# Performance work log

Hardware: AMD Instinct MI355X
Metric: run time of the kernel (lower is better)

The kernel has to match this reference:

```python
import jax, jax.numpy as jnp
import numpy as np


def setup_inputs() -> dict:
    key = jax.random.key(0)
    x = jax.random.normal(key, (8, 2048, 512), dtype=jnp.float32)
    return {"x": x}


def reference(x):
    # x: [B, S, D]; unscaled causal self-attention with Q=K=V=x
    B, S, D = x.shape
    scores = jnp.einsum('bsd,btd->bst', x, x)  # [B, S, S]
    causal = jnp.tril(jnp.ones((S, S), dtype=bool))  # True where allowed
    scores = jnp.where(causal[None, :, :], scores, -jnp.inf)
    attn = jax.nn.softmax(scores, axis=-1)
    out = jnp.einsum('bst,btd->bsd', attn, x)  # [B, S, D]
    return out
```

## Files before the change

### kernel.cpp

```cpp
#include <hip/hip_runtime.h>


#define S_LEN 2048
#define D_DIM 512
#define BATCH_ELEMS 1048576

typedef short s16x8 __attribute__((ext_vector_type(8)));
typedef float f32x4 __attribute__((ext_vector_type(4)));

__device__ __forceinline__ unsigned short f2b_rne(float f) {
  unsigned int u = __float_as_uint(f);
  return (unsigned short)((u + 0x7FFFu + ((u >> 16) & 1u)) >> 16);
}
__device__ __forceinline__ unsigned short f2b_fast(float f) {
  return (unsigned short)((__float_as_uint(f) + 0x8000u) >> 16);
}

template <int CTRL>
__device__ __forceinline__ float dppf(float x) {
  return __uint_as_float((unsigned)__builtin_amdgcn_update_dpp(
      0, (int)__float_as_uint(x), CTRL, 0xF, 0xF, true));
}
__device__ __forceinline__ float red16_max(float v) {
  v = fmaxf(v, dppf<0xB1>(v));
  v = fmaxf(v, dppf<0x4E>(v));
  v = fmaxf(v, dppf<0x124>(v));
  v = fmaxf(v, dppf<0x128>(v));
  return v;
}
__device__ __forceinline__ float red16_sum(float v) {
  v += dppf<0xB1>(v);
  v += dppf<0x4E>(v);
  v += dppf<0x124>(v);
  v += dppf<0x128>(v);
  return v;
}

__global__ void pack_kernel(const float* __restrict__ x,
                            unsigned short* __restrict__ Kf,
                            unsigned short* __restrict__ Vf) {
  __shared__ unsigned short A[64 * 72];
  __shared__ unsigned short T[64 * 72];
  const int bid = blockIdx.x;
  const int b = bid >> 8, rem = bid & 255;
  const int s0 = (rem >> 3) * 64, d0 = (rem & 7) * 64;
  const int tid = threadIdx.x;

  #pragma unroll
  for (int it = 0; it < 2; ++it) {
    int slot = it * 256 + tid;
    int row = slot >> 3, c = slot & 7;
    const float* src = x + ((size_t)(b * S_LEN + s0 + row)) * D_DIM + d0 + c * 8;
    const float4 v0 = *(const float4*)(src);
    const float4 v1 = *(const float4*)(src + 4);
    s16x8 o;
    o[0] = (short)f2b_rne(v0.x); o[1] = (short)f2b_rne(v0.y);
    o[2] = (short)f2b_rne(v0.z); o[3] = (short)f2b_rne(v0.w);
    o[4] = (short)f2b_rne(v1.x); o[5] = (short)f2b_rne(v1.y);
    o[6] = (short)f2b_rne(v1.z); o[7] = (short)f2b_rne(v1.w);
    *(s16x8*)&A[row * 72 + c * 8] = o;
  }
  __syncthreads();

  {
    int sr = tid >> 4, sc = tid & 15;
    ushort4 a0 = *(const ushort4*)&A[(4 * sr + 0) * 72 + 4 * sc];
    ushort4 a1 = *(const ushort4*)&A[(4 * sr + 1) * 72 + 4 * sc];
    ushort4 a2 = *(const ushort4*)&A[(4 * sr + 2) * 72 + 4 * sc];
    ushort4 a3 = *(const ushort4*)&A[(4 * sr + 3) * 72 + 4 * sc];
    ushort4 t0; t0.x = a0.x; t0.y = a1.x; t0.z = a2.x; t0.w = a3.x;
    ushort4 t1; t1.x = a0.y; t1.y = a1.y; t1.z = a2.y; t1.w = a3.y;
    ushort4 t2; t2.x = a0.z; t2.y = a1.z; t2.z = a2.z; t2.w = a3.z;
    ushort4 t3; t3.x = a0.w; t3.y = a1.w; t3.z = a2.w; t3.w = a3.w;
    *(ushort4*)&T[(4 * sc + 0) * 72 + 4 * sr] = t0;
    *(ushort4*)&T[(4 * sc + 1) * 72 + 4 * sr] = t1;
    *(ushort4*)&T[(4 * sc + 2) * 72 + 4 * sr] = t2;
    *(ushort4*)&T[(4 * sc + 3) * 72 + 4 * sr] = t3;
  }
  __syncthreads();

  #pragma unroll
  for (int it = 0; it < 2; ++it) {
    int slot = it * 256 + tid;
    int frag = slot >> 6;
    int lane = slot & 63;
    int l15 = lane & 15, quad = lane >> 4;
    int f1 = frag >> 1, f0 = frag & 1;
    {
      s16x8 val = *(const s16x8*)&A[(f1 * 16 + l15) * 72 + f0 * 32 + quad * 8];
      size_t kg = (size_t)(s0 >> 4) + f1, db = (size_t)(d0 >> 5) + f0;
      *(s16x8*)(Kf + (size_t)b * BATCH_ELEMS + (kg * 16 + db) * 512 + lane * 8) = val;
    }
    {
      s16x8 val = *(const s16x8*)&T[(f1 * 16 + l15) * 72 + f0 * 32 + quad * 8];
      size_t dg = (size_t)(d0 >> 4) + f1, kb = (size_t)(s0 >> 5) + f0;
      *(s16x8*)(Vf + (size_t)b * BATCH_ELEMS + (dg * 64 + kb) * 512 + lane * 8) = val;
    }
  }
}

__global__ __launch_bounds__(256, 2)
void attn_kernel(const unsigned short* __restrict__ Kf,
                 const unsigned short* __restrict__ Vf,
                 float* __restrict__ out) {
  __shared__ unsigned short ldsK[16384];
  __shared__ float Xc[4][512];
  __shared__ unsigned short Pw[4][16 * 40];

  const int bid = blockIdx.x;
  const int bat = bid & 7;
  const int t = (bid < 256) ? (63 - (bid >> 3)) : ((bid - 256) >> 3);
  const int q0 = t * 32;
  const int tid = threadIdx.x;
  const int w = tid >> 6;
  const int pairIdx = w >> 1;
  const int wip = w & 1;
  const int lane = tid & 63;
  const int l15 = lane & 15, quad = lane >> 4;
  const size_t batOff = (size_t)bat * BATCH_ELEMS;

  auto stageK = [&](int kt) {
    const unsigned short* ks =
        Kf + batOff + (size_t)kt * 16384 + (size_t)(w * 8) * 512 + lane * 8;
    #pragma unroll
    for (int i = 0; i < 8; ++i) {
      __builtin_amdgcn_global_load_lds(
          (const __attribute__((address_space(1))) unsigned int*)(ks + i * 512),
          (__attribute__((address_space(3))) unsigned int*)&ldsK[(w * 8 + i) * 512],
          16, 0, 0);
    }
  };

  s16x8 vreg[16];
  auto loadV = [&](int kt) {
    const unsigned short* vb = Vf + batOff + (size_t)kt * 512 + lane * 8;
    #pragma unroll
    for (int dgl = 0; dgl < 16; ++dgl) {
      int dg = wip * 16 + dgl;
      vreg[dgl] = *(const s16x8*)(vb + (size_t)dg * 32768);
    }
  };

  stageK(0);
  loadV(0);

  s16x8 qf[8];
  {
    const unsigned short* qb =
        Kf + batOff + ((size_t)(2 * t + pairIdx) * 16 + wip * 8) * 512 + lane * 8;
    #pragma unroll
    for (int i = 0; i < 8; ++i) qf[i] = *(const s16x8*)(qb + i * 512);
  }

  f32x4 O[16];
  float m[4], l[4];
  #pragma unroll
  for (int n = 0; n < 16; ++n) O[n] = (f32x4){0.f, 0.f, 0.f, 0.f};
  #pragma unroll
  for (int r = 0; r < 4; ++r) { m[r] = -3e38f; l[r] = 0.f; }

  __syncthreads();

  for (int kt = 0; kt <= t; ++kt) {
    f32x4 sacc[2];
    sacc[0] = (f32x4){0.f, 0.f, 0.f, 0.f};
    sacc[1] = (f32x4){0.f, 0.f, 0.f, 0.f};
    __builtin_amdgcn_s_setprio(1);
    #pragma unroll
    for (int i = 0; i < 8; ++i) {
      int db = wip * 8 + i;
      s16x8 k0 = *(const s16x8*)&ldsK[db * 512 + lane * 8];
      s16x8 k1 = *(const s16x8*)&ldsK[(16 + db) * 512 + lane * 8];
      sacc[0] = __builtin_amdgcn_mfma_f32_16x16x32_bf16(qf[i], k0, sacc[0], 0, 0, 0);
      sacc[1] = __builtin_amdgcn_mfma_f32_16x16x32_bf16(qf[i], k1, sacc[1], 0, 0, 0);
    }
    __builtin_amdgcn_s_setprio(0);

    *(f32x4*)&Xc[w][lane * 4] = sacc[0];
    *(f32x4*)&Xc[w][256 + lane * 4] = sacc[1];
    __syncthreads();
    {
      f32x4 pc0 = *(const f32x4*)&Xc[w ^ 1][lane * 4];
      f32x4 pc1 = *(const f32x4*)&Xc[w ^ 1][256 + lane * 4];
      sacc[0] += pc0;
      sacc[1] += pc1;
    }

    if (kt < t) stageK(kt + 1);

    if (kt == t) {
      #pragma unroll
      for (int kg2 = 0; kg2 < 2; ++kg2)
        #pragma unroll
        for (int r = 0; r < 4; ++r) {
          int key = kt * 32 + kg2 * 16 + l15;
          int row = q0 + 16 * pairIdx + quad * 4 + r;
          if (key > row) sacc[kg2][r] = -3e38f;
        }
    }

    float mt[4], alpha[4];
    #pragma unroll
    for (int r = 0; r < 4; ++r)
      mt[r] = red16_max(fmaxf(sacc[0][r], sacc[1][r]));
    bool needAny = (mt[0] > m[0]) | (mt[1] > m[1]) | (mt[2] > m[2]) | (mt[3] > m[3]);
    unsigned long long bal = __ballot(needAny);
    if (bal) {
      #pragma unroll
      for (int r = 0; r < 4; ++r) {
        float mn = fmaxf(m[r], mt[r]);
        alpha[r] = __expf(m[r] - mn);
        m[r] = mn;
      }
    } else {
      #pragma unroll
      for (int r = 0; r < 4; ++r) alpha[r] = 1.0f;
    }
    float p[2][4];
    #pragma unroll
    for (int kg2 = 0; kg2 < 2; ++kg2)
      #pragma unroll
      for (int r = 0; r < 4; ++r) p[kg2][r] = __expf(sacc[kg2][r] - m[r]);
    #pragma unroll
    for (int r = 0; r < 4; ++r)
      l[r] = l[r] * alpha[r] + red16_sum(p[0][r] + p[1][r]);

    #pragma unroll
    for (int kg2 = 0; kg2 < 2; ++kg2)
      #pragma unroll
      for (int r = 0; r < 4; ++r)
        Pw[w][(quad * 4 + r) * 40 + kg2 * 16 + l15] = f2b_fast(p[kg2][r]);
    s16x8 pa = *(const s16x8*)&Pw[w][l15 * 40 + quad * 8];

    if (bal) {
      #pragma unroll
      for (int n = 0; n < 16; ++n)
        #pragma unroll
        for (int r = 0; r < 4; ++r) O[n][r] *= alpha[r];
    }

    __builtin_amdgcn_s_setprio(1);
    #pragma unroll
    for (int dgl = 0; dgl < 16; ++dgl)
      O[dgl] = __builtin_amdgcn_mfma_f32_16x16x32_bf16(pa, vreg[dgl], O[dgl], 0, 0, 0);
    __builtin_amdgcn_s_setprio(0);

    if (kt < t) loadV(kt + 1);

    __syncthreads();
  }

  float invl[4];
  #pragma unroll
  for (int r = 0; r < 4; ++r) invl[r] = 1.0f / l[r];
  float* ob = out + ((size_t)(bat * S_LEN + q0 + 16 * pairIdx)) * D_DIM + wip * 256;
  #pragma unroll
  for (int dgl = 0; dgl < 16; ++dgl)
    #pragma unroll
    for (int r = 0; r < 4; ++r)
      ob[(size_t)(quad * 4 + r) * D_DIM + dgl * 16 + l15] = O[dgl][r] * invl[r];
}

extern "C" void kernel_launch(void* const* d_in, const int* in_sizes, int n_in,
                              void* d_out, int out_size, void* d_ws, size_t ws_size,
                              hipStream_t stream) {
  (void)in_sizes; (void)n_in; (void)out_size; (void)ws_size;
  const float* x = (const float*)d_in[0];
  float* out = (float*)d_out;
  unsigned short* Kf = (unsigned short*)d_ws;
  unsigned short* Vf = (unsigned short*)((char*)d_ws + (16u << 20));
  pack_kernel<<<2048, 256, 0, stream>>>(x, Kf, Vf);
  attn_kernel<<<512, 256, 0, stream>>>(Kf, Vf, out);
}
```

Before: 191.4 us.

## Split query tiles to 16 rows per block with 4-way D-split partial scores

Each block now handles 16 query rows instead of 32, and all four waves split the D dimension four ways for both the QK dot product and the PV output, reducing partial scores across four LDS slots. The grid doubles to 1024 blocks, with blocks ordered longest-first by row group. The block-wide __syncthreads calls become raw s_barrier with explicit waitcnt so the next V loads can stay in flight across the barrier. The aim is more parallelism and fewer registers per thread. The cost is that each K tile staged in LDS is now shared by only 16 query rows, which doubles K/V traffic per unit of work, and the partial-score reduction does more LDS reads.

```diff
diff --git a/kernel.cpp b/kernel.cpp
--- a/kernel.cpp
+++ b/kernel.cpp
@@ -109,12 +109,11 @@
 
   const int bid = blockIdx.x;
   const int bat = bid & 7;
-  const int t = (bid < 256) ? (63 - (bid >> 3)) : ((bid - 256) >> 3);
-  const int q0 = t * 32;
+  const int rg = 127 - (bid >> 3);
+  const int q0 = rg * 16;
+  const int tmax = rg >> 1;
   const int tid = threadIdx.x;
   const int w = tid >> 6;
-  const int pairIdx = w >> 1;
-  const int wip = w & 1;
   const int lane = tid & 63;
   const int l15 = lane & 15, quad = lane >> 4;
   const size_t batOff = (size_t)bat * BATCH_ELEMS;
@@ -131,44 +130,42 @@
     }
   };
 
-  s16x8 vreg[16];
+  s16x8 vreg[8];
   auto loadV = [&](int kt) {
     const unsigned short* vb = Vf + batOff + (size_t)kt * 512 + lane * 8;
     #pragma unroll
-    for (int dgl = 0; dgl < 16; ++dgl) {
-      int dg = wip * 16 + dgl;
-      vreg[dgl] = *(const s16x8*)(vb + (size_t)dg * 32768);
-    }
+    for (int dgl = 0; dgl < 8; ++dgl)
+      vreg[dgl] = *(const s16x8*)(vb + (size_t)(w * 8 + dgl) * 32768);
   };
 
   stageK(0);
   loadV(0);
 
-  s16x8 qf[8];
+  s16x8 qf[4];
   {
     const unsigned short* qb =
-        Kf + batOff + ((size_t)(2 * t + pairIdx) * 16 + wip * 8) * 512 + lane * 8;
-    #pragma unroll
-    for (int i = 0; i < 8; ++i) qf[i] = *(const s16x8*)(qb + i * 512);
-  }
-
-  f32x4 O[16];
+        Kf + batOff + ((size_t)rg * 16 + w * 4) * 512 + lane * 8;
+    #pragma unroll
+    for (int i = 0; i < 4; ++i) qf[i] = *(const s16x8*)(qb + i * 512);
+  }
+
+  f32x4 O[8];
   float m[4], l[4];
   #pragma unroll
-  for (int n = 0; n < 16; ++n) O[n] = (f32x4){0.f, 0.f, 0.f, 0.f};
+  for (int n = 0; n < 8; ++n) O[n] = (f32x4){0.f, 0.f, 0.f, 0.f};
   #pragma unroll
   for (int r = 0; r < 4; ++r) { m[r] = -3e38f; l[r] = 0.f; }
 
   __syncthreads();
 
-  for (int kt = 0; kt <= t; ++kt) {
+  for (int kt = 0;; ++kt) {
     f32x4 sacc[2];
     sacc[0] = (f32x4){0.f, 0.f, 0.f, 0.f};
     sacc[1] = (f32x4){0.f, 0.f, 0.f, 0.f};
     __builtin_amdgcn_s_setprio(1);
     #pragma unroll
-    for (int i = 0; i < 8; ++i) {
-      int db = wip * 8 + i;
+    for (int i = 0; i < 4; ++i) {
+      int db = w * 4 + i;
       s16x8 k0 = *(const s16x8*)&ldsK[db * 512 + lane * 8];
       s16x8 k1 = *(const s16x8*)&ldsK[(16 + db) * 512 + lane * 8];
       sacc[0] = __builtin_amdgcn_mfma_f32_16x16x32_bf16(qf[i], k0, sacc[0], 0, 0, 0);
@@ -178,23 +175,31 @@
 
     *(f32x4*)&Xc[w][lane * 4] = sacc[0];
     *(f32x4*)&Xc[w][256 + lane * 4] = sacc[1];
-    __syncthreads();
+    asm volatile("s_waitcnt lgkmcnt(0)" ::: "memory");
+    __builtin_amdgcn_s_barrier();
+    __builtin_amdgcn_sched_barrier(0);
     {
-      f32x4 pc0 = *(const f32x4*)&Xc[w ^ 1][lane * 4];
-      f32x4 pc1 = *(const f32x4*)&Xc[w ^ 1][256 + lane * 4];
-      sacc[0] += pc0;
-      sacc[1] += pc1;
-    }
-
-    if (kt < t) stageK(kt + 1);
-
-    if (kt == t) {
+      f32x4 s0 = *(const f32x4*)&Xc[0][lane * 4];
+      s0 += *(const f32x4*)&Xc[1][lane * 4];
+      s0 += *(const f32x4*)&Xc[2][lane * 4];
+      s0 += *(const f32x4*)&Xc[3][lane * 4];
+      f32x4 s1 = *(const f32x4*)&Xc[0][256 + lane * 4];
+      s1 += *(const f32x4*)&Xc[1][256 + lane * 4];
+      s1 += *(const f32x4*)&Xc[2][256 + lane * 4];
+      s1 += *(const f32x4*)&Xc[3][256 + lane * 4];
+      sacc[0] = s0;
+      sacc[1] = s1;
+    }
+
+    if (kt < tmax) stageK(kt + 1);
+
+    if (kt == tmax) {
       #pragma unroll
       for (int kg2 = 0; kg2 < 2; ++kg2)
         #pragma unroll
         for (int r = 0; r < 4; ++r) {
           int key = kt * 32 + kg2 * 16 + l15;
-          int row = q0 + 16 * pairIdx + quad * 4 + r;
+          int row = q0 + quad * 4 + r;
           if (key > row) sacc[kg2][r] = -3e38f;
         }
     }
@@ -234,28 +239,32 @@
 
     if (bal) {
       #pragma unroll
-      for (int n = 0; n < 16; ++n)
+      for (int n = 0; n < 8; ++n)
         #pragma unroll
         for (int r = 0; r < 4; ++r) O[n][r] *= alpha[r];
     }
 
     __builtin_amdgcn_s_setprio(1);
     #pragma unroll
-    for (int dgl = 0; dgl < 16; ++dgl)
+    for (int dgl = 0; dgl < 8; ++dgl)
       O[dgl] = __builtin_amdgcn_mfma_f32_16x16x32_bf16(pa, vreg[dgl], O[dgl], 0, 0, 0);
     __builtin_amdgcn_s_setprio(0);
 
-    if (kt < t) loadV(kt + 1);
-
-    __syncthreads();
+    if (kt == tmax) break;
+
+    loadV(kt + 1);
+
+    asm volatile("s_waitcnt vmcnt(8)" ::: "memory");
+    __builtin_amdgcn_s_barrier();
+    __builtin_amdgcn_sched_barrier(0);
   }
 
   float invl[4];
   #pragma unroll
   for (int r = 0; r < 4; ++r) invl[r] = 1.0f / l[r];
-  float* ob = out + ((size_t)(bat * S_LEN + q0 + 16 * pairIdx)) * D_DIM + wip * 256;
-  #pragma unroll
-  for (int dgl = 0; dgl < 16; ++dgl)
+  float* ob = out + ((size_t)(bat * S_LEN + q0)) * D_DIM + w * 128;
+  #pragma unroll
+  for (int dgl = 0; dgl < 8; ++dgl)
     #pragma unroll
     for (int r = 0; r < 4; ++r)
       ob[(size_t)(quad * 4 + r) * D_DIM + dgl * 16 + l15] = O[dgl][r] * invl[r];
@@ -270,5 +279,5 @@
   unsigned short* Kf = (unsigned short*)d_ws;
   unsigned short* Vf = (unsigned short*)((char*)d_ws + (16u << 20));
   pack_kernel<<<2048, 256, 0, stream>>>(x, Kf, Vf);
-  attn_kernel<<<512, 256, 0, stream>>>(Kf, Vf, out);
-}
+  attn_kernel<<<1024, 256, 0, stream>>>(Kf, Vf, out);
+}
```

New measurement: 180.5 us. -5.7%, faster.
